# Kernel tuning notes

Measured on AMD Instinct MI355X. Metric: run time of the kernel, lower is better.

## Reference

```python
import jax, jax.numpy as jnp
import numpy as np

N_PAPER, N_AUTHOR = 50000, 25000
D_PAPER, D_AUTHOR = 256, 128
HID, OUT = 256, 256
E = 400000


def setup_inputs() -> dict:
    key = jax.random.key(0)
    ks = iter(jax.random.split(key, 64))

    def w(shape, fan_in):
        return jax.random.normal(next(ks), shape, jnp.float32) / np.float32(np.sqrt(fan_in))

    inp = {
        "x_paper": jax.random.normal(next(ks), (N_PAPER, D_PAPER), jnp.float32),
        "x_author": jax.random.normal(next(ks), (N_AUTHOR, D_AUTHOR), jnp.float32),
        "cites_src": jax.random.randint(next(ks), (E,), 0, N_PAPER, jnp.int32),
        "cites_dst": jax.random.randint(next(ks), (E,), 0, N_PAPER, jnp.int32),
        "writes_src": jax.random.randint(next(ks), (E,), 0, N_AUTHOR, jnp.int32),
        "writes_dst": jax.random.randint(next(ks), (E,), 0, N_PAPER, jnp.int32),
        "rev_src": jax.random.randint(next(ks), (E,), 0, N_PAPER, jnp.int32),
        "rev_dst": jax.random.randint(next(ks), (E,), 0, N_AUTHOR, jnp.int32),
        # layer 1 params: per edge type, SAGEConv lin_l (src->hid, bias) + lin_r (dst->hid, no bias)
        "l1_cites_Wl": w((D_PAPER, HID), D_PAPER), "l1_cites_bl": w((HID,), HID), "l1_cites_Wr": w((D_PAPER, HID), D_PAPER),
        "l1_writes_Wl": w((D_AUTHOR, HID), D_AUTHOR), "l1_writes_bl": w((HID,), HID), "l1_writes_Wr": w((D_PAPER, HID), D_PAPER),
        "l1_rev_Wl": w((D_PAPER, HID), D_PAPER), "l1_rev_bl": w((HID,), HID), "l1_rev_Wr": w((D_AUTHOR, HID), D_AUTHOR),
        # layer 2 params: all inputs are HID wide
        "l2_cites_Wl": w((HID, OUT), HID), "l2_cites_bl": w((OUT,), OUT), "l2_cites_Wr": w((HID, OUT), HID),
        "l2_writes_Wl": w((HID, OUT), HID), "l2_writes_bl": w((OUT,), OUT), "l2_writes_Wr": w((HID, OUT), HID),
        "l2_rev_Wl": w((HID, OUT), HID), "l2_rev_bl": w((OUT,), OUT), "l2_rev_Wr": w((HID, OUT), HID),
    }
    return inp


def _sage(x_src, x_dst, src, dst, Wl, bl, Wr, n_dst):
    # mean aggregation of source features over incoming edges per dst node
    msg = jax.ops.segment_sum(x_src[src], dst, num_segments=n_dst)          # [n_dst, d_src]
    cnt = jax.ops.segment_sum(jnp.ones(src.shape, x_src.dtype), dst, num_segments=n_dst)
    mean = msg / jnp.maximum(cnt, 1.0)[:, None]
    # SAGEConv: lin_l(aggregated) + lin_r(x_dst); bias on lin_l only
    return mean @ Wl + bl + x_dst @ Wr


def reference(x_paper, x_author,
              cites_src, cites_dst, writes_src, writes_dst, rev_src, rev_dst,
              l1_cites_Wl, l1_cites_bl, l1_cites_Wr,
              l1_writes_Wl, l1_writes_bl, l1_writes_Wr,
              l1_rev_Wl, l1_rev_bl, l1_rev_Wr,
              l2_cites_Wl, l2_cites_bl, l2_cites_Wr,
              l2_writes_Wl, l2_writes_bl, l2_writes_Wr,
              l2_rev_Wl, l2_rev_bl, l2_rev_Wr):
    # layer 1: HeteroConv sums contributions from edge types sharing a dst type
    p1 = (_sage(x_paper, x_paper, cites_src, cites_dst, l1_cites_Wl, l1_cites_bl, l1_cites_Wr, N_PAPER)
          + _sage(x_author, x_paper, writes_src, writes_dst, l1_writes_Wl, l1_writes_bl, l1_writes_Wr, N_PAPER))
    a1 = _sage(x_paper, x_author, rev_src, rev_dst, l1_rev_Wl, l1_rev_bl, l1_rev_Wr, N_AUTHOR)
    p1 = jax.nn.relu(p1)
    a1 = jax.nn.relu(a1)
    # layer 2
    p2 = (_sage(p1, p1, cites_src, cites_dst, l2_cites_Wl, l2_cites_bl, l2_cites_Wr, N_PAPER)
          + _sage(a1, p1, writes_src, writes_dst, l2_writes_Wl, l2_writes_bl, l2_writes_Wr, N_PAPER))
    a2 = _sage(p1, a1, rev_src, rev_dst, l2_rev_Wl, l2_rev_bl, l2_rev_Wr, N_AUTHOR)
    return (p2, a2)
```

## Files before the change

### kernel.cpp

```cpp
#include <hip/hip_runtime.h>
#include <cstdint>
#include <cstddef>

#define DEVFN static __device__ __forceinline__

typedef __attribute__((ext_vector_type(8))) short shortx8;
typedef __attribute__((ext_vector_type(4))) float floatx4;

DEVFN float bf2f(unsigned short u) {
  union { unsigned int i; float f; } v; v.i = ((unsigned int)u) << 16; return v.f;
}
DEVFN unsigned short f2bf(float f) {
  union { float f; unsigned int i; } v; v.f = f;
  unsigned int r = v.i + 0x7FFFu + ((v.i >> 16) & 1u);
  return (unsigned short)(r >> 16);
}

DEVFN void gload_lds16(const void* g, void* l) {
  __builtin_amdgcn_global_load_lds(
      (const __attribute__((address_space(1))) void*)(uintptr_t)g,
      (__attribute__((address_space(3))) void*)(uint32_t)(uintptr_t)l,
      16, 0, 0);
}


__global__ void count_edges(const int* __restrict__ dc, const int* __restrict__ dw,
                            const int* __restrict__ dr,
                            int* cntC, int* cntW, int* cntR, int E_) {
  int i = blockIdx.x * blockDim.x + threadIdx.x;
  const int stride = gridDim.x * blockDim.x;
  for (; i < 3 * E_; i += stride) {
    if (i < E_)            atomicAdd(&cntC[dc[i]], 1);
    else if (i < 2 * E_)   atomicAdd(&cntW[dw[i - E_]], 1);
    else                   atomicAdd(&cntR[dr[i - 2 * E_]], 1);
  }
}

__global__ __launch_bounds__(256)
void scan_pass1(const int* __restrict__ cC, int nC,
                const int* __restrict__ cW, int nW,
                const int* __restrict__ cR, int nR,
                int* __restrict__ bs, int nbC, int nbW) {
  const int b = blockIdx.x;
  const int* cnt; int n, lb, bsoff;
  if (b < nbC)            { cnt = cC; n = nC; lb = b;             bsoff = 0; }
  else if (b < nbC + nbW) { cnt = cW; n = nW; lb = b - nbC;       bsoff = nbC; }
  else                    { cnt = cR; n = nR; lb = b - nbC - nbW; bsoff = nbC + nbW; }
  const int t = threadIdx.x, lane = t & 63, wid = t >> 6;
  const int base = lb * 1024 + t * 4;
  int c0 = 0, c1 = 0, c2 = 0, c3 = 0;
  if (base + 3 < n) { int4 q = *(const int4*)(cnt + base); c0 = q.x; c1 = q.y; c2 = q.z; c3 = q.w; }
  else {
    if (base < n)     c0 = cnt[base];
    if (base + 1 < n) c1 = cnt[base + 1];
    if (base + 2 < n) c2 = cnt[base + 2];
  }
  int v = c0 + c1 + c2 + c3;
  for (int off = 32; off; off >>= 1) v += __shfl_xor(v, off, 64);
  __shared__ int wsum[4];
  if (lane == 0) wsum[wid] = v;
  __syncthreads();
  if (t == 0) bs[bsoff + lb] = wsum[0] + wsum[1] + wsum[2] + wsum[3];
}

__global__ __launch_bounds__(256)
void scan_pass2(int* __restrict__ cC, int* __restrict__ rC, float* __restrict__ vC, int nC,
                int* __restrict__ cW, int* __restrict__ rW, float* __restrict__ vW, int nW,
                int* __restrict__ cR, int* __restrict__ rR, float* __restrict__ vR, int nR,
                const int* __restrict__ bs, int nbC, int nbW, int nbR) {
  const int b = blockIdx.x;
  int* cnt; int* rp; float* inv; int n, lb, bsoff, nb;
  if (b < nbC)            { cnt = cC; rp = rC; inv = vC; n = nC; lb = b;             bsoff = 0;         nb = nbC; }
  else if (b < nbC + nbW) { cnt = cW; rp = rW; inv = vW; n = nW; lb = b - nbC;       bsoff = nbC;       nb = nbW; }
  else                    { cnt = cR; rp = rR; inv = vR; n = nR; lb = b - nbC - nbW; bsoff = nbC + nbW; nb = nbR; }
  const int t = threadIdx.x, lane = t & 63, wid = t >> 6;
  __shared__ int sh_off;
  __shared__ int wsum[4];
  if (wid == 0) {
    int v = (lane < lb) ? bs[bsoff + lane] : 0;
    for (int off = 32; off; off >>= 1) v += __shfl_xor(v, off, 64);
    if (lane == 0) sh_off = v;
  }
  const int base = lb * 1024 + t * 4;
  int c0 = 0, c1 = 0, c2 = 0, c3 = 0;
  if (base + 3 < n) { int4 q = *(const int4*)(cnt + base); c0 = q.x; c1 = q.y; c2 = q.z; c3 = q.w; }
  else {
    if (base < n)     c0 = cnt[base];
    if (base + 1 < n) c1 = cnt[base + 1];
    if (base + 2 < n) c2 = cnt[base + 2];
  }
  const int tsum = c0 + c1 + c2 + c3;
  int isc = tsum;
  for (int off = 1; off < 64; off <<= 1) {
    int y = __shfl_up(isc, off, 64);
    if (lane >= off) isc += y;
  }
  if (lane == 63) wsum[wid] = isc;
  __syncthreads();
  int woff = sh_off;
  for (int w = 0; w < wid; ++w) woff += wsum[w];
  const int e = woff + isc - tsum;
  const int ex0 = e, ex1 = e + c0, ex2 = e + c0 + c1, ex3 = e + c0 + c1 + c2;
  if (base + 3 < n) {
    *(int4*)(rp + base) = make_int4(ex0, ex1, ex2, ex3);
    *(int4*)(cnt + base) = make_int4(ex0, ex1, ex2, ex3);
    *(float4*)(inv + base) = make_float4(1.f / (c0 > 1 ? c0 : 1), 1.f / (c1 > 1 ? c1 : 1),
                                         1.f / (c2 > 1 ? c2 : 1), 1.f / (c3 > 1 ? c3 : 1));
  } else {
    if (base < n)     { rp[base] = ex0;     cnt[base] = ex0;     inv[base] = 1.f / (c0 > 1 ? c0 : 1); }
    if (base + 1 < n) { rp[base + 1] = ex1; cnt[base + 1] = ex1; inv[base + 1] = 1.f / (c1 > 1 ? c1 : 1); }
    if (base + 2 < n) { rp[base + 2] = ex2; cnt[base + 2] = ex2; inv[base + 2] = 1.f / (c2 > 1 ? c2 : 1); }
  }
  if (lb == nb - 1 && t == 255) rp[n] = woff + isc;
}

__global__ void fill_edges(const int* __restrict__ sc, const int* __restrict__ dc,
                           const int* __restrict__ sw, const int* __restrict__ dw,
                           const int* __restrict__ sr, const int* __restrict__ dr,
                           int* curC, int* curW, int* curR,
                           int* eC, int* eW, int* eR, int E_) {
  int i = blockIdx.x * blockDim.x + threadIdx.x;
  const int stride = gridDim.x * blockDim.x;
  for (; i < 3 * E_; i += stride) {
    if (i < E_)          { int p = atomicAdd(&curC[dc[i]], 1); eC[p] = sc[i]; }
    else if (i < 2 * E_) { int j = i - E_;     int p = atomicAdd(&curW[dw[j]], 1); eW[p] = sw[j]; }
    else                 { int j = i - 2 * E_; int p = atomicAdd(&curR[dr[j]], 1); eR[p] = sr[j]; }
  }
}


__global__ void cvt_bf16(const float4* __restrict__ a, unsigned short* __restrict__ oa, long na4,
                         const float4* __restrict__ b, unsigned short* __restrict__ ob, long nb4) {
  long i = (long)blockIdx.x * blockDim.x + threadIdx.x;
  const long tot = na4 + nb4;
  const long stride = (long)gridDim.x * blockDim.x;
  for (; i < tot; i += stride) {
    const float4* src; unsigned short* dst; long j;
    if (i < na4) { src = a; dst = oa; j = i; } else { src = b; dst = ob; j = i - na4; }
    float4 v = src[j];
    ushort4 o;
    o.x = f2bf(v.x); o.y = f2bf(v.y); o.z = f2bf(v.z); o.w = f2bf(v.w);
    *(ushort4*)(dst + j * 4) = o;
  }
}


__global__ void prep_w(const float* Wl1c, const float* bl1c, const float* Wr1c,
                       const float* Wl1w, const float* bl1w, const float* Wr1w,
                       const float* Wl1r, const float* bl1r, const float* Wr1r,
                       const float* Wl2c, const float* bl2c, const float* Wr2c,
                       const float* Wl2w, const float* bl2w, const float* Wr2w,
                       const float* Wl2r, const float* bl2r, const float* Wr2r,
                       unsigned short* WT, float* bias) {
  const int mat = blockIdx.x >> 8;
  const int nn = blockIdx.x & 255;
  const int t = threadIdx.x;
  if (mat == 0) {
    unsigned short* out = WT + (size_t)nn * 640;
    for (int k = t; k < 640; k += 256) {
      float v;
      if (k < 256)      v = Wl1c[k * 256 + nn];
      else if (k < 384) v = Wl1w[(k - 256) * 256 + nn];
      else              v = Wr1c[(k - 384) * 256 + nn] + Wr1w[(k - 384) * 256 + nn];
      out[k] = f2bf(v);
    }
    if (t == 0) bias[nn] = bl1c[nn] + bl1w[nn];
  } else if (mat == 1) {
    unsigned short* out = WT + (size_t)256 * 640 + (size_t)nn * 384;
    for (int k = t; k < 384; k += 256) {
      float v = (k < 256) ? Wl1r[k * 256 + nn] : Wr1r[(k - 256) * 256 + nn];
      out[k] = f2bf(v);
    }
    if (t == 0) bias[256 + nn] = bl1r[nn];
  } else if (mat == 2) {
    unsigned short* out = WT + (size_t)256 * (640 + 384) + (size_t)nn * 768;
    for (int k = t; k < 768; k += 256) {
      float v;
      if (k < 256)      v = Wl2c[k * 256 + nn];
      else if (k < 512) v = Wl2w[(k - 256) * 256 + nn];
      else              v = Wr2c[(k - 512) * 256 + nn] + Wr2w[(k - 512) * 256 + nn];
      out[k] = f2bf(v);
    }
    if (t == 0) bias[512 + nn] = bl2c[nn] + bl2w[nn];
  } else {
    unsigned short* out = WT + (size_t)256 * (640 + 384 + 768) + (size_t)nn * 512;
    for (int k = t; k < 512; k += 256) {
      float v = (k < 256) ? Wl2r[k * 256 + nn] : Wr2r[(k - 256) * 256 + nn];
      out[k] = f2bf(v);
    }
    if (t == 0) bias[768 + nn] = bl2r[nn];
  }
}


template <int D>
__global__ __launch_bounds__(256)
void agg_mean(const unsigned short* __restrict__ feat, const int* __restrict__ rp,
              const int* __restrict__ es, const float* __restrict__ inv,
              unsigned short* __restrict__ out, int n) {
  const int node = blockIdx.x * 4 + (threadIdx.x >> 6);
  const int lane = threadIdx.x & 63;
  if (node >= n) return;
  const int e0 = rp[node], e1 = rp[node + 1];
  const float sc = inv[node];
  if constexpr (D == 256) {
    const int c0 = lane * 4;
    float a0 = 0, a1 = 0, a2 = 0, a3 = 0;
    int e = e0;
    for (; e + 3 < e1; e += 4) {
      int s0 = es[e], s1 = es[e + 1], s2 = es[e + 2], s3 = es[e + 3];
      ushort4 v0 = *(const ushort4*)(feat + (size_t)s0 * 256 + c0);
      ushort4 v1 = *(const ushort4*)(feat + (size_t)s1 * 256 + c0);
      ushort4 v2 = *(const ushort4*)(feat + (size_t)s2 * 256 + c0);
      ushort4 v3 = *(const ushort4*)(feat + (size_t)s3 * 256 + c0);
      a0 += (bf2f(v0.x) + bf2f(v1.x)) + (bf2f(v2.x) + bf2f(v3.x));
      a1 += (bf2f(v0.y) + bf2f(v1.y)) + (bf2f(v2.y) + bf2f(v3.y));
      a2 += (bf2f(v0.z) + bf2f(v1.z)) + (bf2f(v2.z) + bf2f(v3.z));
      a3 += (bf2f(v0.w) + bf2f(v1.w)) + (bf2f(v2.w) + bf2f(v3.w));
    }
    for (; e < e1; ++e) {
      int s0 = es[e];
      ushort4 v0 = *(const ushort4*)(feat + (size_t)s0 * 256 + c0);
      a0 += bf2f(v0.x); a1 += bf2f(v0.y); a2 += bf2f(v0.z); a3 += bf2f(v0.w);
    }
    ushort4 o;
    o.x = f2bf(a0 * sc); o.y = f2bf(a1 * sc); o.z = f2bf(a2 * sc); o.w = f2bf(a3 * sc);
    *(ushort4*)(out + (size_t)node * 256 + c0) = o;
  } else {
    const int c0 = lane * 2;
    float a0 = 0, a1 = 0;
    int e = e0;
    for (; e + 3 < e1; e += 4) {
      int s0 = es[e], s1 = es[e + 1], s2 = es[e + 2], s3 = es[e + 3];
      ushort2 v0 = *(const ushort2*)(feat + (size_t)s0 * 128 + c0);
      ushort2 v1 = *(const ushort2*)(feat + (size_t)s1 * 128 + c0);
      ushort2 v2 = *(const ushort2*)(feat + (size_t)s2 * 128 + c0);
      ushort2 v3 = *(const ushort2*)(feat + (size_t)s3 * 128 + c0);
      a0 += (bf2f(v0.x) + bf2f(v1.x)) + (bf2f(v2.x) + bf2f(v3.x));
      a1 += (bf2f(v0.y) + bf2f(v1.y)) + (bf2f(v2.y) + bf2f(v3.y));
    }
    for (; e < e1; ++e) {
      int s0 = es[e];
      ushort2 v0 = *(const ushort2*)(feat + (size_t)s0 * 128 + c0);
      a0 += bf2f(v0.x); a1 += bf2f(v0.y);
    }
    ushort2 o; o.x = f2bf(a0 * sc); o.y = f2bf(a1 * sc);
    *(ushort2*)(out + (size_t)node * 128 + c0) = o;
  }
}


struct Segs {
  const unsigned short *p0, *p1, *p2;
  int ld0, ld1, ld2;
  int ke0, ke1;
};

template <int KTOT, bool RELU, bool OBF16>
__global__ __launch_bounds__(256, 2)
void gemm_sage(Segs sg, const unsigned short* __restrict__ Wt,
               const float* __restrict__ bias, void* __restrict__ outp, int M) {
  __shared__ alignas(16) unsigned short lsA[128 * 64];
  __shared__ alignas(16) unsigned short lsB[128 * 64];

  const int tid = threadIdx.x;
  const int lane = tid & 63;
  const int wave = tid >> 6;
  const int wr = wave >> 1, wc = wave & 1;
  const int mt = blockIdx.x >> 1, nt = blockIdx.x & 1;

  const floatx4 fzero = {0.f, 0.f, 0.f, 0.f};
  floatx4 acc[4][4];
#pragma unroll
  for (int m = 0; m < 4; ++m)
#pragma unroll
    for (int n = 0; n < 4; ++n) acc[m][n] = fzero;

  const int srow = tid >> 3;
  const int scol = (tid & 7) * 8;
  const int arow = wr * 64 + (lane & 15);
  const int brow = wc * 64 + (lane & 15);
  const int kq = (lane >> 4) * 8;

  constexpr int KT = KTOT / 64;
#pragma unroll 1
  for (int kt = 0; kt < KT; ++kt) {
    const int k0 = kt * 64;
    const unsigned short* sp; int sld, skb;
    if (k0 < sg.ke0)      { sp = sg.p0; sld = sg.ld0; skb = 0; }
    else if (k0 < sg.ke1) { sp = sg.p1; sld = sg.ld1; skb = sg.ke0; }
    else                  { sp = sg.p2; sld = sg.ld2; skb = sg.ke1; }

#pragma unroll
    for (int s = 0; s < 4; ++s) {
      int r = s * 32 + srow;
      int g = mt * 128 + r; g = g < M ? g : M - 1;
      gload_lds16(sp + (size_t)g * sld + (k0 - skb) + scol, lsA + r * 64 + scol);
    }
#pragma unroll
    for (int s = 0; s < 4; ++s) {
      int r = s * 32 + srow;
      gload_lds16(Wt + (size_t)(nt * 128 + r) * KTOT + k0 + scol, lsB + r * 64 + scol);
    }
    __syncthreads();

    shortx8 af[2][4], bq[2][4];
#pragma unroll
    for (int kk = 0; kk < 2; ++kk)
#pragma unroll
      for (int i = 0; i < 4; ++i) {
        af[kk][i] = *(const shortx8*)(lsA + (arow + i * 16) * 64 + kk * 32 + kq);
        bq[kk][i] = *(const shortx8*)(lsB + (brow + i * 16) * 64 + kk * 32 + kq);
      }
#pragma unroll
    for (int m = 0; m < 4; ++m)
#pragma unroll
      for (int n = 0; n < 4; ++n) {
        acc[m][n] = __builtin_amdgcn_mfma_f32_16x16x32_bf16(af[0][m], bq[0][n], acc[m][n], 0, 0, 0);
        acc[m][n] = __builtin_amdgcn_mfma_f32_16x16x32_bf16(af[1][m], bq[1][n], acc[m][n], 0, 0, 0);
      }
    __syncthreads();
  }

  const int lr = (lane >> 4) * 4;
  const int lc = lane & 15;
  const int rb = mt * 128 + wr * 64;
  const int cb = nt * 128 + wc * 64;
#pragma unroll
  for (int m = 0; m < 4; ++m) {
#pragma unroll
    for (int j = 0; j < 4; ++j) {
      const int row = rb + m * 16 + lr + j;
      if (row < M) {
#pragma unroll
        for (int n = 0; n < 4; ++n) {
          const int col = cb + n * 16 + lc;
          float v = acc[m][n][j] + bias[col];
          if (RELU) v = v > 0.f ? v : 0.f;
          if (OBF16) ((unsigned short*)outp)[(size_t)row * 256 + col] = f2bf(v);
          else       ((float*)outp)[(size_t)row * 256 + col] = v;
        }
      }
    }
  }
}


extern "C" void kernel_launch(void* const* d_in, const int* in_sizes, int n_in,
                              void* d_out, int out_size, void* d_ws, size_t ws_size,
                              hipStream_t stream) {
  const float* x_paper = (const float*)d_in[0];
  const float* x_author = (const float*)d_in[1];
  const int* cites_src = (const int*)d_in[2];
  const int* cites_dst = (const int*)d_in[3];
  const int* writes_src = (const int*)d_in[4];
  const int* writes_dst = (const int*)d_in[5];
  const int* rev_src = (const int*)d_in[6];
  const int* rev_dst = (const int*)d_in[7];
  const float* Wl1c = (const float*)d_in[8];  const float* bl1c = (const float*)d_in[9];  const float* Wr1c = (const float*)d_in[10];
  const float* Wl1w = (const float*)d_in[11]; const float* bl1w = (const float*)d_in[12]; const float* Wr1w = (const float*)d_in[13];
  const float* Wl1r = (const float*)d_in[14]; const float* bl1r = (const float*)d_in[15]; const float* Wr1r = (const float*)d_in[16];
  const float* Wl2c = (const float*)d_in[17]; const float* bl2c = (const float*)d_in[18]; const float* Wr2c = (const float*)d_in[19];
  const float* Wl2w = (const float*)d_in[20]; const float* bl2w = (const float*)d_in[21]; const float* Wr2w = (const float*)d_in[22];
  const float* Wl2r = (const float*)d_in[23]; const float* bl2r = (const float*)d_in[24]; const float* Wr2r = (const float*)d_in[25];

  const int NP = in_sizes[0] / 256;
  const int NA = in_sizes[1] / 128;
  const int E = in_sizes[2];

  char* w = (char*)d_ws;
  auto alloc = [&](size_t bytes) -> char* {
    char* p = w;
    w += (bytes + 255) & ~(size_t)255;
    return p;
  };

  unsigned short* xpb = (unsigned short*)alloc((size_t)NP * 256 * 2);
  unsigned short* xab = (unsigned short*)alloc((size_t)NA * 128 * 2);
  unsigned short* mA  = (unsigned short*)alloc((size_t)NP * 256 * 2);
  unsigned short* mB  = (unsigned short*)alloc((size_t)NP * 256 * 2);
  unsigned short* mC  = (unsigned short*)alloc((size_t)NA * 256 * 2);
  unsigned short* p1b = (unsigned short*)alloc((size_t)NP * 256 * 2);
  unsigned short* a1b = (unsigned short*)alloc((size_t)NA * 256 * 2);
  unsigned short* WT  = (unsigned short*)alloc((size_t)2304 * 256 * 2);
  float* bias = (float*)alloc(4 * 256 * 4);
  int* curC = (int*)alloc((size_t)NP * 4);
  int* curW = (int*)alloc((size_t)NP * 4);
  int* curR = (int*)alloc((size_t)NA * 4);
  int* rpC = (int*)alloc((size_t)(NP + 1) * 4);
  int* rpW = (int*)alloc((size_t)(NP + 1) * 4);
  int* rpR = (int*)alloc((size_t)(NA + 1) * 4);
  float* invC = (float*)alloc((size_t)NP * 4);
  float* invW = (float*)alloc((size_t)NP * 4);
  float* invR = (float*)alloc((size_t)NA * 4);
  int* esC = (int*)alloc((size_t)E * 4);
  int* esW = (int*)alloc((size_t)E * 4);
  int* esR = (int*)alloc((size_t)E * 4);
  int* bsums = (int*)alloc(256 * 4);

  hipMemsetAsync(curC, 0, (size_t)NP * 4, stream);
  hipMemsetAsync(curW, 0, (size_t)NP * 4, stream);
  hipMemsetAsync(curR, 0, (size_t)NA * 4, stream);

  prep_w<<<1024, 256, 0, stream>>>(Wl1c, bl1c, Wr1c, Wl1w, bl1w, Wr1w, Wl1r, bl1r, Wr1r,
                                   Wl2c, bl2c, Wr2c, Wl2w, bl2w, Wr2w, Wl2r, bl2r, Wr2r,
                                   WT, bias);
  cvt_bf16<<<2048, 256, 0, stream>>>((const float4*)x_paper, xpb, (long)NP * 256 / 4,
                                     (const float4*)x_author, xab, (long)NA * 128 / 4);

  const int nbC = (NP + 1023) / 1024, nbW = (NP + 1023) / 1024, nbR = (NA + 1023) / 1024;
  count_edges<<<2048, 256, 0, stream>>>(cites_dst, writes_dst, rev_dst, curC, curW, curR, E);
  scan_pass1<<<nbC + nbW + nbR, 256, 0, stream>>>(curC, NP, curW, NP, curR, NA, bsums, nbC, nbW);
  scan_pass2<<<nbC + nbW + nbR, 256, 0, stream>>>(curC, rpC, invC, NP, curW, rpW, invW, NP,
                                                  curR, rpR, invR, NA, bsums, nbC, nbW, nbR);
  fill_edges<<<2048, 256, 0, stream>>>(cites_src, cites_dst, writes_src, writes_dst, rev_src, rev_dst,
                                       curC, curW, curR, esC, esW, esR, E);

  agg_mean<256><<<(NP + 3) / 4, 256, 0, stream>>>(xpb, rpC, esC, invC, mA, NP);
  agg_mean<128><<<(NP + 3) / 4, 256, 0, stream>>>(xab, rpW, esW, invW, mB, NP);
  agg_mean<256><<<(NA + 3) / 4, 256, 0, stream>>>(xpb, rpR, esR, invR, mC, NA);

  {
    Segs s; s.p0 = mA; s.ld0 = 256; s.ke0 = 256;
    s.p1 = mB; s.ld1 = 128; s.ke1 = 384;
    s.p2 = xpb; s.ld2 = 256;
    gemm_sage<640, true, true><<<((NP + 127) / 128) * 2, 256, 0, stream>>>(s, WT, bias, p1b, NP);
  }
  {
    Segs s; s.p0 = mC; s.ld0 = 256; s.ke0 = 256;
    s.p1 = xab; s.ld1 = 128; s.ke1 = 384;
    s.p2 = xab; s.ld2 = 128;
    gemm_sage<384, true, true><<<((NA + 127) / 128) * 2, 256, 0, stream>>>(
        s, WT + (size_t)256 * 640, bias + 256, a1b, NA);
  }

  agg_mean<256><<<(NP + 3) / 4, 256, 0, stream>>>(p1b, rpC, esC, invC, mA, NP);
  agg_mean<256><<<(NP + 3) / 4, 256, 0, stream>>>(a1b, rpW, esW, invW, mB, NP);
  agg_mean<256><<<(NA + 3) / 4, 256, 0, stream>>>(p1b, rpR, esR, invR, mC, NA);

  {
    Segs s; s.p0 = mA; s.ld0 = 256; s.ke0 = 256;
    s.p1 = mB; s.ld1 = 256; s.ke1 = 512;
    s.p2 = p1b; s.ld2 = 256;
    gemm_sage<768, false, false><<<((NP + 127) / 128) * 2, 256, 0, stream>>>(
        s, WT + (size_t)256 * (640 + 384), bias + 512, d_out, NP);
  }
  {
    Segs s; s.p0 = mC; s.ld0 = 256; s.ke0 = 256;
    s.p1 = a1b; s.ld1 = 256; s.ke1 = 512;
    s.p2 = a1b; s.ld2 = 256;
    gemm_sage<512, false, false><<<((NA + 127) / 128) * 2, 256, 0, stream>>>(
        s, WT + (size_t)256 * (640 + 384 + 768), bias + 768,
        (float*)d_out + (size_t)NP * 256, NA);
  }
}
```

Measured before the change: 603.4 us.

## Build CSR with range-owned LDS histograms and fuse preprocessing and aggregation launches

Replaces the global-atomic edge count and fill kernels with 64 blocks that each own a contiguous range of destination nodes. Each block scans all edges and does its atomics in shared memory, which removes the memsets and the contention on global atomics. In exchange, every block rereads the full edge arrays. Weight prep and bf16 conversion are merged into one launch, the three per-layer mean-aggregation launches become one multi-job kernel each, and the gather loop is unrolled to 8 edges for more memory-level parallelism.

```diff
diff --git a/kernel.cpp b/kernel.cpp
--- a/kernel.cpp
+++ b/kernel.cpp
@@ -24,17 +24,91 @@
 }
 
 
-__global__ void count_edges(const int* __restrict__ dc, const int* __restrict__ dw,
-                            const int* __restrict__ dr,
-                            int* cntC, int* cntW, int* cntR, int E_) {
-  int i = blockIdx.x * blockDim.x + threadIdx.x;
-  const int stride = gridDim.x * blockDim.x;
-  for (; i < 3 * E_; i += stride) {
-    if (i < E_)            atomicAdd(&cntC[dc[i]], 1);
-    else if (i < 2 * E_)   atomicAdd(&cntW[dw[i - E_]], 1);
-    else                   atomicAdd(&cntR[dr[i - 2 * E_]], 1);
-  }
-}
+__global__ __launch_bounds__(1024)
+void count_own(const int* __restrict__ dc, const int* __restrict__ dw,
+               const int* __restrict__ dr,
+               int* __restrict__ cntC, int* __restrict__ cntW, int* __restrict__ cntR,
+               int E_, int NP_, int NA_) {
+  const int b = blockIdx.x, t = threadIdx.x;
+  const int loP = (int)((long)b * NP_ / 64), hiP = (int)((long)(b + 1) * NP_ / 64);
+  const int loA = (int)((long)b * NA_ / 64), hiA = (int)((long)(b + 1) * NA_ / 64);
+  const int nP = hiP - loP, nA = hiA - loA;
+  __shared__ int hC[784], hW[784], hR[392];
+  for (int i = t; i < 784; i += 1024) { hC[i] = 0; hW[i] = 0; }
+  for (int i = t; i < 392; i += 1024) hR[i] = 0;
+  __syncthreads();
+  const int E4 = E_ & ~3;
+  for (int i = t * 4; i + 3 < E_; i += 4096) {
+    int4 d = *(const int4*)(dc + i);
+    if (d.x >= loP && d.x < hiP) atomicAdd(&hC[d.x - loP], 1);
+    if (d.y >= loP && d.y < hiP) atomicAdd(&hC[d.y - loP], 1);
+    if (d.z >= loP && d.z < hiP) atomicAdd(&hC[d.z - loP], 1);
+    if (d.w >= loP && d.w < hiP) atomicAdd(&hC[d.w - loP], 1);
+  }
+  for (int i = E4 + t; i < E_; i += 1024) { int d = dc[i]; if (d >= loP && d < hiP) atomicAdd(&hC[d - loP], 1); }
+  for (int i = t * 4; i + 3 < E_; i += 4096) {
+    int4 d = *(const int4*)(dw + i);
+    if (d.x >= loP && d.x < hiP) atomicAdd(&hW[d.x - loP], 1);
+    if (d.y >= loP && d.y < hiP) atomicAdd(&hW[d.y - loP], 1);
+    if (d.z >= loP && d.z < hiP) atomicAdd(&hW[d.z - loP], 1);
+    if (d.w >= loP && d.w < hiP) atomicAdd(&hW[d.w - loP], 1);
+  }
+  for (int i = E4 + t; i < E_; i += 1024) { int d = dw[i]; if (d >= loP && d < hiP) atomicAdd(&hW[d - loP], 1); }
+  for (int i = t * 4; i + 3 < E_; i += 4096) {
+    int4 d = *(const int4*)(dr + i);
+    if (d.x >= loA && d.x < hiA) atomicAdd(&hR[d.x - loA], 1);
+    if (d.y >= loA && d.y < hiA) atomicAdd(&hR[d.y - loA], 1);
+    if (d.z >= loA && d.z < hiA) atomicAdd(&hR[d.z - loA], 1);
+    if (d.w >= loA && d.w < hiA) atomicAdd(&hR[d.w - loA], 1);
+  }
+  for (int i = E4 + t; i < E_; i += 1024) { int d = dr[i]; if (d >= loA && d < hiA) atomicAdd(&hR[d - loA], 1); }
+  __syncthreads();
+  for (int i = t; i < nP; i += 1024) { cntC[loP + i] = hC[i]; cntW[loP + i] = hW[i]; }
+  for (int i = t; i < nA; i += 1024) cntR[loA + i] = hR[i];
+}
+
+__global__ __launch_bounds__(1024)
+void fill_own(const int* __restrict__ sc, const int* __restrict__ dc,
+              const int* __restrict__ sw, const int* __restrict__ dw,
+              const int* __restrict__ sr, const int* __restrict__ dr,
+              const int* __restrict__ rpC, const int* __restrict__ rpW, const int* __restrict__ rpR,
+              int* __restrict__ eC, int* __restrict__ eW, int* __restrict__ eR,
+              int E_, int NP_, int NA_) {
+  const int b = blockIdx.x, t = threadIdx.x;
+  const int loP = (int)((long)b * NP_ / 64), hiP = (int)((long)(b + 1) * NP_ / 64);
+  const int loA = (int)((long)b * NA_ / 64), hiA = (int)((long)(b + 1) * NA_ / 64);
+  const int nP = hiP - loP, nA = hiA - loA;
+  __shared__ int cC[784], cW[784], cR[392];
+  for (int i = t; i < nP; i += 1024) { cC[i] = rpC[loP + i]; cW[i] = rpW[loP + i]; }
+  for (int i = t; i < nA; i += 1024) cR[i] = rpR[loA + i];
+  __syncthreads();
+  const int E4 = E_ & ~3;
+  for (int i = t * 4; i + 3 < E_; i += 4096) {
+    int4 d = *(const int4*)(dc + i);
+    if (d.x >= loP && d.x < hiP) { int p = atomicAdd(&cC[d.x - loP], 1); eC[p] = sc[i]; }
+    if (d.y >= loP && d.y < hiP) { int p = atomicAdd(&cC[d.y - loP], 1); eC[p] = sc[i + 1]; }
+    if (d.z >= loP && d.z < hiP) { int p = atomicAdd(&cC[d.z - loP], 1); eC[p] = sc[i + 2]; }
+    if (d.w >= loP && d.w < hiP) { int p = atomicAdd(&cC[d.w - loP], 1); eC[p] = sc[i + 3]; }
+  }
+  for (int i = E4 + t; i < E_; i += 1024) { int d = dc[i]; if (d >= loP && d < hiP) { int p = atomicAdd(&cC[d - loP], 1); eC[p] = sc[i]; } }
+  for (int i = t * 4; i + 3 < E_; i += 4096) {
+    int4 d = *(const int4*)(dw + i);
+    if (d.x >= loP && d.x < hiP) { int p = atomicAdd(&cW[d.x - loP], 1); eW[p] = sw[i]; }
+    if (d.y >= loP && d.y < hiP) { int p = atomicAdd(&cW[d.y - loP], 1); eW[p] = sw[i + 1]; }
+    if (d.z >= loP && d.z < hiP) { int p = atomicAdd(&cW[d.z - loP], 1); eW[p] = sw[i + 2]; }
+    if (d.w >= loP && d.w < hiP) { int p = atomicAdd(&cW[d.w - loP], 1); eW[p] = sw[i + 3]; }
+  }
+  for (int i = E4 + t; i < E_; i += 1024) { int d = dw[i]; if (d >= loP && d < hiP) { int p = atomicAdd(&cW[d - loP], 1); eW[p] = sw[i]; } }
+  for (int i = t * 4; i + 3 < E_; i += 4096) {
+    int4 d = *(const int4*)(dr + i);
+    if (d.x >= loA && d.x < hiA) { int p = atomicAdd(&cR[d.x - loA], 1); eR[p] = sr[i]; }
+    if (d.y >= loA && d.y < hiA) { int p = atomicAdd(&cR[d.y - loA], 1); eR[p] = sr[i + 1]; }
+    if (d.z >= loA && d.z < hiA) { int p = atomicAdd(&cR[d.z - loA], 1); eR[p] = sr[i + 2]; }
+    if (d.w >= loA && d.w < hiA) { int p = atomicAdd(&cR[d.w - loA], 1); eR[p] = sr[i + 3]; }
+  }
+  for (int i = E4 + t; i < E_; i += 1024) { int d = dr[i]; if (d >= loA && d < hiA) { int p = atomicAdd(&cR[d - loA], 1); eR[p] = sr[i]; } }
+}
+
 
 __global__ __launch_bounds__(256)
 void scan_pass1(const int* __restrict__ cC, int nC,
@@ -64,12 +138,12 @@
 }
 
 __global__ __launch_bounds__(256)
-void scan_pass2(int* __restrict__ cC, int* __restrict__ rC, float* __restrict__ vC, int nC,
-                int* __restrict__ cW, int* __restrict__ rW, float* __restrict__ vW, int nW,
-                int* __restrict__ cR, int* __restrict__ rR, float* __restrict__ vR, int nR,
+void scan_pass2(const int* __restrict__ cC, int* __restrict__ rC, float* __restrict__ vC, int nC,
+                const int* __restrict__ cW, int* __restrict__ rW, float* __restrict__ vW, int nW,
+                const int* __restrict__ cR, int* __restrict__ rR, float* __restrict__ vR, int nR,
                 const int* __restrict__ bs, int nbC, int nbW, int nbR) {
   const int b = blockIdx.x;
-  int* cnt; int* rp; float* inv; int n, lb, bsoff, nb;
+  const int* cnt; int* rp; float* inv; int n, lb, bsoff, nb;
   if (b < nbC)            { cnt = cC; rp = rC; inv = vC; n = nC; lb = b;             bsoff = 0;         nb = nbC; }
   else if (b < nbC + nbW) { cnt = cW; rp = rW; inv = vW; n = nW; lb = b - nbC;       bsoff = nbC;       nb = nbW; }
   else                    { cnt = cR; rp = rR; inv = vR; n = nR; lb = b - nbC - nbW; bsoff = nbC + nbW; nb = nbR; }
@@ -103,58 +177,44 @@
   const int ex0 = e, ex1 = e + c0, ex2 = e + c0 + c1, ex3 = e + c0 + c1 + c2;
   if (base + 3 < n) {
     *(int4*)(rp + base) = make_int4(ex0, ex1, ex2, ex3);
-    *(int4*)(cnt + base) = make_int4(ex0, ex1, ex2, ex3);
     *(float4*)(inv + base) = make_float4(1.f / (c0 > 1 ? c0 : 1), 1.f / (c1 > 1 ? c1 : 1),
                                          1.f / (c2 > 1 ? c2 : 1), 1.f / (c3 > 1 ? c3 : 1));
   } else {
-    if (base < n)     { rp[base] = ex0;     cnt[base] = ex0;     inv[base] = 1.f / (c0 > 1 ? c0 : 1); }
-    if (base + 1 < n) { rp[base + 1] = ex1; cnt[base + 1] = ex1; inv[base + 1] = 1.f / (c1 > 1 ? c1 : 1); }
-    if (base + 2 < n) { rp[base + 2] = ex2; cnt[base + 2] = ex2; inv[base + 2] = 1.f / (c2 > 1 ? c2 : 1); }
+    if (base < n)     { rp[base] = ex0;     inv[base] = 1.f / (c0 > 1 ? c0 : 1); }
+    if (base + 1 < n) { rp[base + 1] = ex1; inv[base + 1] = 1.f / (c1 > 1 ? c1 : 1); }
+    if (base + 2 < n) { rp[base + 2] = ex2; inv[base + 2] = 1.f / (c2 > 1 ? c2 : 1); }
   }
   if (lb == nb - 1 && t == 255) rp[n] = woff + isc;
 }
 
-__global__ void fill_edges(const int* __restrict__ sc, const int* __restrict__ dc,
-                           const int* __restrict__ sw, const int* __restrict__ dw,
-                           const int* __restrict__ sr, const int* __restrict__ dr,
-                           int* curC, int* curW, int* curR,
-                           int* eC, int* eW, int* eR, int E_) {
-  int i = blockIdx.x * blockDim.x + threadIdx.x;
-  const int stride = gridDim.x * blockDim.x;
-  for (; i < 3 * E_; i += stride) {
-    if (i < E_)          { int p = atomicAdd(&curC[dc[i]], 1); eC[p] = sc[i]; }
-    else if (i < 2 * E_) { int j = i - E_;     int p = atomicAdd(&curW[dw[j]], 1); eW[p] = sw[j]; }
-    else                 { int j = i - 2 * E_; int p = atomicAdd(&curR[dr[j]], 1); eR[p] = sr[j]; }
-  }
-}
-
-
-__global__ void cvt_bf16(const float4* __restrict__ a, unsigned short* __restrict__ oa, long na4,
-                         const float4* __restrict__ b, unsigned short* __restrict__ ob, long nb4) {
-  long i = (long)blockIdx.x * blockDim.x + threadIdx.x;
-  const long tot = na4 + nb4;
-  const long stride = (long)gridDim.x * blockDim.x;
-  for (; i < tot; i += stride) {
-    const float4* src; unsigned short* dst; long j;
-    if (i < na4) { src = a; dst = oa; j = i; } else { src = b; dst = ob; j = i - na4; }
-    float4 v = src[j];
-    ushort4 o;
-    o.x = f2bf(v.x); o.y = f2bf(v.y); o.z = f2bf(v.z); o.w = f2bf(v.w);
-    *(ushort4*)(dst + j * 4) = o;
-  }
-}
-
-
-__global__ void prep_w(const float* Wl1c, const float* bl1c, const float* Wr1c,
-                       const float* Wl1w, const float* bl1w, const float* Wr1w,
-                       const float* Wl1r, const float* bl1r, const float* Wr1r,
-                       const float* Wl2c, const float* bl2c, const float* Wr2c,
-                       const float* Wl2w, const float* bl2w, const float* Wr2w,
-                       const float* Wl2r, const float* bl2r, const float* Wr2r,
-                       unsigned short* WT, float* bias) {
+
+__global__ __launch_bounds__(256)
+void prep_all(const float* Wl1c, const float* bl1c, const float* Wr1c,
+              const float* Wl1w, const float* bl1w, const float* Wr1w,
+              const float* Wl1r, const float* bl1r, const float* Wr1r,
+              const float* Wl2c, const float* bl2c, const float* Wr2c,
+              const float* Wl2w, const float* bl2w, const float* Wr2w,
+              const float* Wl2r, const float* bl2r, const float* Wr2r,
+              unsigned short* WT, float* bias,
+              const float4* __restrict__ xp, unsigned short* __restrict__ oxp, long np4,
+              const float4* __restrict__ xa, unsigned short* __restrict__ oxa, long na4) {
+  const int t = threadIdx.x;
+  if (blockIdx.x >= 1024) {
+    long i = (long)(blockIdx.x - 1024) * 256 + t;
+    const long tot = np4 + na4;
+    const long stride = (long)(gridDim.x - 1024) * 256;
+    for (; i < tot; i += stride) {
+      const float4* src; unsigned short* dst; long j;
+      if (i < np4) { src = xp; dst = oxp; j = i; } else { src = xa; dst = oxa; j = i - np4; }
+      float4 v = src[j];
+      ushort4 o;
+      o.x = f2bf(v.x); o.y = f2bf(v.y); o.z = f2bf(v.z); o.w = f2bf(v.w);
+      *(ushort4*)(dst + j * 4) = o;
+    }
+    return;
+  }
   const int mat = blockIdx.x >> 8;
   const int nn = blockIdx.x & 255;
-  const int t = threadIdx.x;
   if (mat == 0) {
     unsigned short* out = WT + (size_t)nn * 640;
     for (int k = t; k < 640; k += 256) {
@@ -194,25 +254,38 @@
 
 
 template <int D>
-__global__ __launch_bounds__(256)
-void agg_mean(const unsigned short* __restrict__ feat, const int* __restrict__ rp,
-              const int* __restrict__ es, const float* __restrict__ inv,
-              unsigned short* __restrict__ out, int n) {
-  const int node = blockIdx.x * 4 + (threadIdx.x >> 6);
-  const int lane = threadIdx.x & 63;
-  if (node >= n) return;
-  const int e0 = rp[node], e1 = rp[node + 1];
-  const float sc = inv[node];
+DEVFN void agg_node(const unsigned short* __restrict__ feat, const int* __restrict__ es,
+                    int e0, int e1, float sc, unsigned short* __restrict__ outrow, int lane) {
   if constexpr (D == 256) {
-    const int c0 = lane * 4;
+    const unsigned short* f = feat + lane * 4;
     float a0 = 0, a1 = 0, a2 = 0, a3 = 0;
     int e = e0;
+    for (; e + 7 < e1; e += 8) {
+      int s0 = es[e], s1 = es[e + 1], s2 = es[e + 2], s3 = es[e + 3];
+      int s4 = es[e + 4], s5 = es[e + 5], s6 = es[e + 6], s7 = es[e + 7];
+      ushort4 v0 = *(const ushort4*)(f + (size_t)s0 * 256);
+      ushort4 v1 = *(const ushort4*)(f + (size_t)s1 * 256);
+      ushort4 v2 = *(const ushort4*)(f + (size_t)s2 * 256);
+      ushort4 v3 = *(const ushort4*)(f + (size_t)s3 * 256);
+      ushort4 v4 = *(const ushort4*)(f + (size_t)s4 * 256);
+      ushort4 v5 = *(const ushort4*)(f + (size_t)s5 * 256);
+      ushort4 v6 = *(const ushort4*)(f + (size_t)s6 * 256);
+      ushort4 v7 = *(const ushort4*)(f + (size_t)s7 * 256);
+      a0 += ((bf2f(v0.x) + bf2f(v1.x)) + (bf2f(v2.x) + bf2f(v3.x))) +
+            ((bf2f(v4.x) + bf2f(v5.x)) + (bf2f(v6.x) + bf2f(v7.x)));
+      a1 += ((bf2f(v0.y) + bf2f(v1.y)) + (bf2f(v2.y) + bf2f(v3.y))) +
+            ((bf2f(v4.y) + bf2f(v5.y)) + (bf2f(v6.y) + bf2f(v7.y)));
+      a2 += ((bf2f(v0.z) + bf2f(v1.z)) + (bf2f(v2.z) + bf2f(v3.z))) +
+            ((bf2f(v4.z) + bf2f(v5.z)) + (bf2f(v6.z) + bf2f(v7.z)));
+      a3 += ((bf2f(v0.w) + bf2f(v1.w)) + (bf2f(v2.w) + bf2f(v3.w))) +
+            ((bf2f(v4.w) + bf2f(v5.w)) + (bf2f(v6.w) + bf2f(v7.w)));
+    }
     for (; e + 3 < e1; e += 4) {
       int s0 = es[e], s1 = es[e + 1], s2 = es[e + 2], s3 = es[e + 3];
-      ushort4 v0 = *(const ushort4*)(feat + (size_t)s0 * 256 + c0);
-      ushort4 v1 = *(const ushort4*)(feat + (size_t)s1 * 256 + c0);
-      ushort4 v2 = *(const ushort4*)(feat + (size_t)s2 * 256 + c0);
-      ushort4 v3 = *(const ushort4*)(feat + (size_t)s3 * 256 + c0);
+      ushort4 v0 = *(const ushort4*)(f + (size_t)s0 * 256);
+      ushort4 v1 = *(const ushort4*)(f + (size_t)s1 * 256);
+      ushort4 v2 = *(const ushort4*)(f + (size_t)s2 * 256);
+      ushort4 v3 = *(const ushort4*)(f + (size_t)s3 * 256);
       a0 += (bf2f(v0.x) + bf2f(v1.x)) + (bf2f(v2.x) + bf2f(v3.x));
       a1 += (bf2f(v0.y) + bf2f(v1.y)) + (bf2f(v2.y) + bf2f(v3.y));
       a2 += (bf2f(v0.z) + bf2f(v1.z)) + (bf2f(v2.z) + bf2f(v3.z));
@@ -220,33 +293,85 @@
     }
     for (; e < e1; ++e) {
       int s0 = es[e];
-      ushort4 v0 = *(const ushort4*)(feat + (size_t)s0 * 256 + c0);
+      ushort4 v0 = *(const ushort4*)(f + (size_t)s0 * 256);
       a0 += bf2f(v0.x); a1 += bf2f(v0.y); a2 += bf2f(v0.z); a3 += bf2f(v0.w);
     }
     ushort4 o;
     o.x = f2bf(a0 * sc); o.y = f2bf(a1 * sc); o.z = f2bf(a2 * sc); o.w = f2bf(a3 * sc);
-    *(ushort4*)(out + (size_t)node * 256 + c0) = o;
+    *(ushort4*)(outrow + lane * 4) = o;
   } else {
-    const int c0 = lane * 2;
+    const unsigned short* f = feat + lane * 2;
     float a0 = 0, a1 = 0;
     int e = e0;
+    for (; e + 7 < e1; e += 8) {
+      int s0 = es[e], s1 = es[e + 1], s2 = es[e + 2], s3 = es[e + 3];
+      int s4 = es[e + 4], s5 = es[e + 5], s6 = es[e + 6], s7 = es[e + 7];
+      ushort2 v0 = *(const ushort2*)(f + (size_t)s0 * 128);
+      ushort2 v1 = *(const ushort2*)(f + (size_t)s1 * 128);
+      ushort2 v2 = *(const ushort2*)(f + (size_t)s2 * 128);
+      ushort2 v3 = *(const ushort2*)(f + (size_t)s3 * 128);
+      ushort2 v4 = *(const ushort2*)(f + (size_t)s4 * 128);
+      ushort2 v5 = *(const ushort2*)(f + (size_t)s5 * 128);
+      ushort2 v6 = *(const ushort2*)(f + (size_t)s6 * 128);
+      ushort2 v7 = *(const ushort2*)(f + (size_t)s7 * 128);
+      a0 += ((bf2f(v0.x) + bf2f(v1.x)) + (bf2f(v2.x) + bf2f(v3.x))) +
+            ((bf2f(v4.x) + bf2f(v5.x)) + (bf2f(v6.x) + bf2f(v7.x)));
+      a1 += ((bf2f(v0.y) + bf2f(v1.y)) + (bf2f(v2.y) + bf2f(v3.y))) +
+            ((bf2f(v4.y) + bf2f(v5.y)) + (bf2f(v6.y) + bf2f(v7.y)));
+    }
     for (; e + 3 < e1; e += 4) {
       int s0 = es[e], s1 = es[e + 1], s2 = es[e + 2], s3 = es[e + 3];
-      ushort2 v0 = *(const ushort2*)(feat + (size_t)s0 * 128 + c0);
-      ushort2 v1 = *(const ushort2*)(feat + (size_t)s1 * 128 + c0);
-      ushort2 v2 = *(const ushort2*)(feat + (size_t)s2 * 128 + c0);
-      ushort2 v3 = *(const ushort2*)(feat + (size_t)s3 * 128 + c0);
+      ushort2 v0 = *(const ushort2*)(f + (size_t)s0 * 128);
+      ushort2 v1 = *(const ushort2*)(f + (size_t)s1 * 128);
+      ushort2 v2 = *(const ushort2*)(f + (size_t)s2 * 128);
+      ushort2 v3 = *(const ushort2*)(f + (size_t)s3 * 128);
       a0 += (bf2f(v0.x) + bf2f(v1.x)) + (bf2f(v2.x) + bf2f(v3.x));
       a1 += (bf2f(v0.y) + bf2f(v1.y)) + (bf2f(v2.y) + bf2f(v3.y));
     }
     for (; e < e1; ++e) {
       int s0 = es[e];
-      ushort2 v0 = *(const ushort2*)(feat + (size_t)s0 * 128 + c0);
+      ushort2 v0 = *(const ushort2*)(f + (size_t)s0 * 128);
       a0 += bf2f(v0.x); a1 += bf2f(v0.y);
     }
     ushort2 o; o.x = f2bf(a0 * sc); o.y = f2bf(a1 * sc);
-    *(ushort2*)(out + (size_t)node * 128 + c0) = o;
-  }
+    *(ushort2*)(outrow + lane * 2) = o;
+  }
+}
+
+struct AggJob {
+  const unsigned short* feat; const int* rp; const int* es; const float* inv;
+  unsigned short* out; int n;
+};
+
+__global__ __launch_bounds__(256)
+void agg_l1(AggJob j0, AggJob j1, AggJob j2, int b0, int b1) {
+  const int b = blockIdx.x;
+  const AggJob* j; int lb; bool d128 = false;
+  if (b < b0)           { j = &j0; lb = b; }
+  else if (b < b0 + b1) { j = &j1; lb = b - b0; }
+  else                  { j = &j2; lb = b - b0 - b1; d128 = true; }
+  const int node = lb * 4 + (threadIdx.x >> 6);
+  const int lane = threadIdx.x & 63;
+  if (node >= j->n) return;
+  const int e0 = j->rp[node], e1 = j->rp[node + 1];
+  const float sc = j->inv[node];
+  if (!d128) agg_node<256>(j->feat, j->es, e0, e1, sc, j->out + (size_t)node * 256, lane);
+  else       agg_node<128>(j->feat, j->es, e0, e1, sc, j->out + (size_t)node * 128, lane);
+}
+
+__global__ __launch_bounds__(256)
+void agg_l2(AggJob j0, AggJob j1, AggJob j2, int b0, int b1) {
+  const int b = blockIdx.x;
+  const AggJob* j; int lb;
+  if (b < b0)           { j = &j0; lb = b; }
+  else if (b < b0 + b1) { j = &j1; lb = b - b0; }
+  else                  { j = &j2; lb = b - b0 - b1; }
+  const int node = lb * 4 + (threadIdx.x >> 6);
+  const int lane = threadIdx.x & 63;
+  if (node >= j->n) return;
+  const int e0 = j->rp[node], e1 = j->rp[node + 1];
+  const float sc = j->inv[node];
+  agg_node<256>(j->feat, j->es, e0, e1, sc, j->out + (size_t)node * 256, lane);
 }
 
 
@@ -384,9 +509,9 @@
   unsigned short* a1b = (unsigned short*)alloc((size_t)NA * 256 * 2);
   unsigned short* WT  = (unsigned short*)alloc((size_t)2304 * 256 * 2);
   float* bias = (float*)alloc(4 * 256 * 4);
-  int* curC = (int*)alloc((size_t)NP * 4);
-  int* curW = (int*)alloc((size_t)NP * 4);
-  int* curR = (int*)alloc((size_t)NA * 4);
+  int* cntC = (int*)alloc((size_t)NP * 4);
+  int* cntW = (int*)alloc((size_t)NP * 4);
+  int* cntR = (int*)alloc((size_t)NA * 4);
   int* rpC = (int*)alloc((size_t)(NP + 1) * 4);
   int* rpW = (int*)alloc((size_t)(NP + 1) * 4);
   int* rpR = (int*)alloc((size_t)(NA + 1) * 4);
@@ -398,27 +523,27 @@
   int* esR = (int*)alloc((size_t)E * 4);
   int* bsums = (int*)alloc(256 * 4);
 
-  hipMemsetAsync(curC, 0, (size_t)NP * 4, stream);
-  hipMemsetAsync(curW, 0, (size_t)NP * 4, stream);
-  hipMemsetAsync(curR, 0, (size_t)NA * 4, stream);
-
-  prep_w<<<1024, 256, 0, stream>>>(Wl1c, bl1c, Wr1c, Wl1w, bl1w, Wr1w, Wl1r, bl1r, Wr1r,
-                                   Wl2c, bl2c, Wr2c, Wl2w, bl2w, Wr2w, Wl2r, bl2r, Wr2r,
-                                   WT, bias);
-  cvt_bf16<<<2048, 256, 0, stream>>>((const float4*)x_paper, xpb, (long)NP * 256 / 4,
+  prep_all<<<2560, 256, 0, stream>>>(Wl1c, bl1c, Wr1c, Wl1w, bl1w, Wr1w, Wl1r, bl1r, Wr1r,
+                                     Wl2c, bl2c, Wr2c, Wl2w, bl2w, Wr2w, Wl2r, bl2r, Wr2r,
+                                     WT, bias,
+                                     (const float4*)x_paper, xpb, (long)NP * 256 / 4,
                                      (const float4*)x_author, xab, (long)NA * 128 / 4);
 
   const int nbC = (NP + 1023) / 1024, nbW = (NP + 1023) / 1024, nbR = (NA + 1023) / 1024;
-  count_edges<<<2048, 256, 0, stream>>>(cites_dst, writes_dst, rev_dst, curC, curW, curR, E);
-  scan_pass1<<<nbC + nbW + nbR, 256, 0, stream>>>(curC, NP, curW, NP, curR, NA, bsums, nbC, nbW);
-  scan_pass2<<<nbC + nbW + nbR, 256, 0, stream>>>(curC, rpC, invC, NP, curW, rpW, invW, NP,
-                                                  curR, rpR, invR, NA, bsums, nbC, nbW, nbR);
-  fill_edges<<<2048, 256, 0, stream>>>(cites_src, cites_dst, writes_src, writes_dst, rev_src, rev_dst,
-                                       curC, curW, curR, esC, esW, esR, E);
-
-  agg_mean<256><<<(NP + 3) / 4, 256, 0, stream>>>(xpb, rpC, esC, invC, mA, NP);
-  agg_mean<128><<<(NP + 3) / 4, 256, 0, stream>>>(xab, rpW, esW, invW, mB, NP);
-  agg_mean<256><<<(NA + 3) / 4, 256, 0, stream>>>(xpb, rpR, esR, invR, mC, NA);
+  count_own<<<64, 1024, 0, stream>>>(cites_dst, writes_dst, rev_dst, cntC, cntW, cntR, E, NP, NA);
+  scan_pass1<<<nbC + nbW + nbR, 256, 0, stream>>>(cntC, NP, cntW, NP, cntR, NA, bsums, nbC, nbW);
+  scan_pass2<<<nbC + nbW + nbR, 256, 0, stream>>>(cntC, rpC, invC, NP, cntW, rpW, invW, NP,
+                                                  cntR, rpR, invR, NA, bsums, nbC, nbW, nbR);
+  fill_own<<<64, 1024, 0, stream>>>(cites_src, cites_dst, writes_src, writes_dst, rev_src, rev_dst,
+                                    rpC, rpW, rpR, esC, esW, esR, E, NP, NA);
+
+  {
+    AggJob j0{xpb, rpC, esC, invC, mA, NP};
+    AggJob j1{xpb, rpR, esR, invR, mC, NA};
+    AggJob j2{xab, rpW, esW, invW, mB, NP};
+    const int b0 = (NP + 3) / 4, b1 = (NA + 3) / 4, b2 = (NP + 3) / 4;
+    agg_l1<<<b0 + b1 + b2, 256, 0, stream>>>(j0, j1, j2, b0, b1);
+  }
 
   {
     Segs s; s.p0 = mA; s.ld0 = 256; s.ke0 = 256;
@@ -434,9 +559,13 @@
         s, WT + (size_t)256 * 640, bias + 256, a1b, NA);
   }
 
-  agg_mean<256><<<(NP + 3) / 4, 256, 0, stream>>>(p1b, rpC, esC, invC, mA, NP);
-  agg_mean<256><<<(NP + 3) / 4, 256, 0, stream>>>(a1b, rpW, esW, invW, mB, NP);
-  agg_mean<256><<<(NA + 3) / 4, 256, 0, stream>>>(p1b, rpR, esR, invR, mC, NA);
+  {
+    AggJob j0{p1b, rpC, esC, invC, mA, NP};
+    AggJob j1{a1b, rpW, esW, invW, mB, NP};
+    AggJob j2{p1b, rpR, esR, invR, mC, NA};
+    const int b0 = (NP + 3) / 4, b1 = (NP + 3) / 4, b2 = (NA + 3) / 4;
+    agg_l2<<<b0 + b1 + b2, 256, 0, stream>>>(j0, j1, j2, b0, b1);
+  }
 
   {
     Segs s; s.p0 = mA; s.ld0 = 256; s.ke0 = 256;
```

After: 917.3 us. 52.0% more time.
